# Kernel optimization log

Hardware: AMD Instinct MI355X
Metric: run time of the kernel (lower is better)

The kernel has to match this reference:

```python
import jax, jax.numpy as jnp
import numpy as np

B, N, C = 8, 1024, 768
H = 12
HD = C // H  # 64
SCALE = C ** (-0.5)  # NOTE: source scales by n_emb^-0.5, not head_dim^-0.5


def setup_inputs() -> dict:
    key = jax.random.key(0)
    k1, k2, k3 = jax.random.split(key, 3)
    x = jax.random.normal(k1, (B, N, C), dtype=jnp.float32)
    W_qkv = jax.random.normal(k2, (C, 3 * C), dtype=jnp.float32) * (C ** -0.5)
    b_qkv = jnp.zeros((3 * C,), dtype=jnp.float32)
    W_proj = jax.random.normal(k3, (C, C), dtype=jnp.float32) * (C ** -0.5)
    b_proj = jnp.zeros((C,), dtype=jnp.float32)
    return {"x": x, "W_qkv": W_qkv, "b_qkv": b_qkv, "W_proj": W_proj, "b_proj": b_proj}


def reference(x, W_qkv, b_qkv, W_proj, b_proj):
    # qkv projection: (B,N,3C) -> (3,B,H,N,HD)
    qkv = x @ W_qkv + b_qkv
    qkv = qkv.reshape(B, N, 3, H, HD).transpose(2, 0, 3, 1, 4)
    q, k, v = qkv[0], qkv[1], qkv[2]
    # scaled dot-product attention (full N x N, as in source)
    attn = jnp.einsum("bhnd,bhmd->bhnm", q, k) * SCALE
    attn = jax.nn.softmax(attn, axis=-1)
    out = jnp.einsum("bhnm,bhmd->bhnd", attn, v)
    out = out.transpose(0, 2, 1, 3).reshape(B, N, C)
    return out @ W_proj + b_proj
```

## Files before the change

### kernel.cpp

```cpp
#include <hip/hip_runtime.h>
#include <hip/hip_bf16.h>
#include <stdint.h>

#define Bb 8
#define Nn_ 1024
#define Cc_ 768
#define Hh 12
#define HDd 64
#define BHh 96
#define SCALE_F 0.03608439182435161f
#define CL2F (0.03608439182435161f * 1.4426950408889634f)
#define THRRAW (3.0f / CL2F)

typedef __attribute__((ext_vector_type(4))) float f32x4;
typedef __attribute__((ext_vector_type(8))) __bf16 bf16x8;

__device__ __forceinline__ unsigned short f2bf(float f) {
  uint32_t u = __builtin_bit_cast(uint32_t, f);
  uint32_t r = (u + 0x7fffu + ((u >> 16) & 1u)) >> 16;
  return (unsigned short)r;
}

__device__ __forceinline__ uint32_t cvtpk(float a, float b) {
  uint32_t r;
  asm("v_cvt_pk_bf16_f32 %0, %1, %2" : "=v"(r) : "v"(a), "v"(b));
  return r;
}

__device__ __forceinline__ f32x4 mfma16(bf16x8 a, bf16x8 b, f32x4 c) {
  return __builtin_amdgcn_mfma_f32_16x16x32_bf16(a, b, c, 0, 0, 0);
}

typedef const __attribute__((address_space(1))) uint32_t* gas1_t;
typedef __attribute__((address_space(3))) uint32_t* las3_t;
__device__ __forceinline__ void gl_lds16(const void* g, void* l) {
  __builtin_amdgcn_global_load_lds((gas1_t)g, (las3_t)l, 16, 0, 0);
}

#define VMCNT(n) asm volatile("s_waitcnt vmcnt(" #n ")" ::: "memory")
#define SBAR() __builtin_amdgcn_s_barrier()
#define SCHED_FENCE() __builtin_amdgcn_sched_barrier(0)

__global__ void k_cvt_x(const float* __restrict__ x, unsigned short* __restrict__ xb, int n4) {
  int i = blockIdx.x * blockDim.x + threadIdx.x;
  if (i >= n4) return;
  float4 v = ((const float4*)x)[i];
  ushort4 o;
  o.x = f2bf(v.x); o.y = f2bf(v.y); o.z = f2bf(v.z); o.w = f2bf(v.w);
  ((ushort4*)xb)[i] = o;
}

template <int R, int CC>
__global__ void k_transpose(const float* __restrict__ src, unsigned short* __restrict__ dst) {
  __shared__ unsigned short tile[64][65];
  int c0 = blockIdx.x * 64;
  int r0 = blockIdx.y * 64;
  int t = threadIdx.x;
#pragma unroll
  for (int i = 0; i < 16; ++i) {
    int idx = t + 256 * i;
    int r = idx >> 6, c = idx & 63;
    tile[r][c] = f2bf(src[(size_t)(r0 + r) * CC + c0 + c]);
  }
  __syncthreads();
#pragma unroll
  for (int i = 0; i < 16; ++i) {
    int idx = t + 256 * i;
    int a = idx >> 6, bq = idx & 63;
    dst[(size_t)(c0 + a) * R + r0 + bq] = tile[bq][a];
  }
}

__global__ __launch_bounds__(256) void k_transpose_v(const unsigned short* __restrict__ V,
                                                     unsigned short* __restrict__ Vt) {
  __shared__ unsigned short tile[64][72];
  int bh = blockIdx.y;
  int n0 = blockIdx.x * 64;
  int t = threadIdx.x;
  const unsigned short* src = V + ((size_t)bh * 1024 + n0) * 64;
#pragma unroll
  for (int i = 0; i < 4; ++i) {
    int idx = t + i * 256;
    int r = idx >> 4, c4 = idx & 15;
    ushort4 v = ((const ushort4*)src)[idx];
    tile[r][c4 * 4 + 0] = v.x; tile[r][c4 * 4 + 1] = v.y;
    tile[r][c4 * 4 + 2] = v.z; tile[r][c4 * 4 + 3] = v.w;
  }
  __syncthreads();
  unsigned short* dst = Vt + (size_t)bh * 64 * 1024 + n0;
#pragma unroll
  for (int i = 0; i < 4; ++i) {
    int idx = t + i * 256;
    int c = idx >> 4, n4 = idx & 15;
    ushort4 o;
    o.x = tile[n4 * 4 + 0][c]; o.y = tile[n4 * 4 + 1][c];
    o.z = tile[n4 * 4 + 2][c]; o.w = tile[n4 * 4 + 3][c];
    ((ushort4*)(dst + (size_t)c * 1024))[n4] = o;
  }
}

template <int EPI, int BMt, int BNt, int MINB>
__global__ __launch_bounds__(256, MINB) void k_gemm(
    const unsigned short* __restrict__ A, const unsigned short* __restrict__ Bt,
    const float* __restrict__ bias, float* __restrict__ out,
    unsigned short* __restrict__ Qb, unsigned short* __restrict__ Kb,
    unsigned short* __restrict__ Vb, int Nw) {
  constexpr int WGM = (BNt == 128) ? 2 : 4;
  constexpr int WM = BMt / WGM;
  constexpr int MR = WM / 16;
  constexpr int AL = BMt / 32;
  constexpr int BL = BNt / 32;
  constexpr int ASZ = BMt * 128;
  constexpr int BUFSZ = ASZ + BNt * 128;
  __shared__ char smem[2 * BUFSZ];
  int t = threadIdx.x;
  int w = t >> 6, lane = t & 63;
  int g = lane >> 4, l15 = lane & 15;
  int bid = blockIdx.x;
  int m0 = ((bid & 7) * 8 + ((bid >> 3) & 7)) * BMt;
  int n0 = (bid >> 6) * BNt;
  int wr = (BNt == 128) ? (w >> 1) : w;
  int wc = (BNt == 128) ? (w & 1) : 0;

  f32x4 acc[MR][4] = {};

  const char* gA[AL];
  const char* gB[BL];
  int sA[AL], sB[BL];
#pragma unroll
  for (int it = 0; it < AL; ++it) {
    int off = it * 4096 + t * 16;
    int row = off >> 7;
    int sb = (off & 127) ^ ((row & 7) << 4);
    gA[it] = (const char*)A + (size_t)(m0 + row) * 1536 + sb;
    sA[it] = it * 4096 + w * 1024;
  }
#pragma unroll
  for (int it = 0; it < BL; ++it) {
    int off = it * 4096 + t * 16;
    int row = off >> 7;
    int sb = (off & 127) ^ ((row & 7) << 4);
    gB[it] = (const char*)Bt + (size_t)(n0 + row) * 1536 + sb;
    sB[it] = ASZ + it * 4096 + w * 1024;
  }

  auto STG = [&](int buf, int kt) {
    char* base = smem + buf * BUFSZ;
#pragma unroll
    for (int it = 0; it < AL; ++it) gl_lds16(gA[it] + kt * 128, base + sA[it]);
#pragma unroll
    for (int it = 0; it < BL; ++it) gl_lds16(gB[it] + kt * 128, base + sB[it]);
  };

  const char *pa[2][MR], *pb[2][4];
#pragma unroll
  for (int ks = 0; ks < 2; ++ks) {
    int kb = ks * 64 + g * 16;
#pragma unroll
    for (int mi = 0; mi < MR; ++mi) {
      int rowA = wr * WM + mi * 16 + l15;
      pa[ks][mi] = smem + rowA * 128 + (kb ^ ((rowA & 7) << 4));
    }
#pragma unroll
    for (int ni = 0; ni < 4; ++ni) {
      int rowB = wc * 64 + ni * 16 + l15;
      pb[ks][ni] = smem + ASZ + rowB * 128 + (kb ^ ((rowB & 7) << 4));
    }
  }

  STG(0, 0);
#pragma unroll
  for (int kt = 0; kt < 12; ++kt) {
    int off = (kt & 1) * BUFSZ;
    if (kt < 11) {
      STG((kt & 1) ^ 1, kt + 1);
      if constexpr (BL == 4) { VMCNT(8); } else { VMCNT(6); }
    } else {
      VMCNT(0);
    }
    SBAR();
    SCHED_FENCE();
    bf16x8 av[2][MR], bv[2][4];
#pragma unroll
    for (int ks = 0; ks < 2; ++ks) {
#pragma unroll
      for (int mi = 0; mi < MR; ++mi) av[ks][mi] = *(const bf16x8*)(pa[ks][mi] + off);
#pragma unroll
      for (int ni = 0; ni < 4; ++ni) bv[ks][ni] = *(const bf16x8*)(pb[ks][ni] + off);
    }
#pragma unroll
    for (int ks = 0; ks < 2; ++ks)
#pragma unroll
      for (int mi = 0; mi < MR; ++mi)
#pragma unroll
        for (int ni = 0; ni < 4; ++ni)
          acc[mi][ni] = mfma16(av[ks][mi], bv[ks][ni], acc[mi][ni]);
    SCHED_FENCE();
    if (kt < 11) SBAR();
  }

#pragma unroll
  for (int mi = 0; mi < MR; ++mi) {
#pragma unroll
    for (int ni = 0; ni < 4; ++ni) {
      int col = n0 + wc * 64 + ni * 16 + l15;
      float bvs = bias[col];
#pragma unroll
      for (int j = 0; j < 4; ++j) {
        int row = m0 + wr * WM + mi * 16 + g * 4 + j;
        float val = acc[mi][ni][j] + bvs;
        if constexpr (EPI == 0) {
          out[(size_t)row * Nw + col] = val;
        } else {
          int bI = row >> 10, n = row & 1023;
          int typ = col / 768, within = col % 768;
          int h = within >> 6, d = within & 63;
          int bh = bI * 12 + h;
          unsigned short bf = f2bf(val);
          unsigned short* dst = (typ == 0) ? Qb : (typ == 1) ? Kb : Vb;
          dst[((size_t)bh * 1024 + n) * 64 + d] = bf;
        }
      }
    }
  }
}

__global__ __launch_bounds__(256, 3) void k_attn(
    const unsigned short* __restrict__ Q, const unsigned short* __restrict__ K,
    const unsigned short* __restrict__ Vt, unsigned short* __restrict__ Oa) {
  __shared__ char smem[49152];
  char* Ks = smem;
  char* Ps = smem + 32768;
  int t = threadIdx.x, w = t >> 6, lane = t & 63;
  int g = lane >> 4, l15 = lane & 15;

  int fb = blockIdx.x;
  int bh = (fb & 7) * 12 + ((fb >> 3) % 12);
  int n0 = (fb / 96) * 128;
  int bI = bh / 12, h = bh % 12;
  char* Pw = Ps + w * 4096;

  bf16x8 qf[2][2];
  {
    const char* qbase = (const char*)Q + ((size_t)bh * 1024 + n0 + w * 32 + l15) * 128 + g * 16;
    qf[0][0] = *(const bf16x8*)(qbase);
    qf[0][1] = *(const bf16x8*)(qbase + 64);
    qf[1][0] = *(const bf16x8*)(qbase + 16 * 128);
    qf[1][1] = *(const bf16x8*)(qbase + 16 * 128 + 64);
  }

  f32x4 acc[2][4] = {};
  float mrun[2] = {-INFINITY, -INFINITY};
  float lrun[2] = {0.f, 0.f};

  const char* pK[2][4];
#pragma unroll
  for (int ks = 0; ks < 2; ++ks)
#pragma unroll
    for (int ff = 0; ff < 4; ++ff) {
      int row = ff * 16 + l15;
      pK[ks][ff] = Ks + row * 128 + ((ks * 64 + g * 16) ^ ((row & 7) << 4));
    }
  char* pPw[2][4];
  const char* pPr[2][2];
#pragma unroll
  for (int q = 0; q < 2; ++q) {
    int prow = q * 16 + l15, swz = (l15 & 7) << 4;
#pragma unroll
    for (int ff = 0; ff < 4; ++ff) pPw[q][ff] = Pw + prow * 128 + ((ff * 32 + g * 8) ^ swz);
#pragma unroll
    for (int ks = 0; ks < 2; ++ks) pPr[q][ks] = Pw + prow * 128 + ((ks * 64 + g * 16) ^ swz);
  }

  int o0 = t * 16, o1 = t * 16 + 4096;
  int r0 = o0 >> 7, r1 = o1 >> 7;
  int sb0 = (o0 & 127) ^ ((r0 & 7) << 4);
  int sb1 = (o1 & 127) ^ ((r1 & 7) << 4);
  const char* KgA = (const char*)K + (size_t)bh * 131072 + (size_t)r0 * 128 + sb0;
  const char* KgB = (const char*)K + (size_t)bh * 131072 + (size_t)r1 * 128 + sb1;
  const char* VgA = (const char*)Vt + (size_t)bh * 131072 + (size_t)r0 * 2048 + sb0;
  const char* VgB = (const char*)Vt + (size_t)bh * 131072 + (size_t)r1 * 2048 + sb1;

  auto STG = [&](int buf, int mt) {
    char* Kd = Ks + buf * 8192;
    char* Vd = Ks + 16384 + buf * 8192;
    gl_lds16(KgA + (size_t)mt * 8192, Kd + w * 1024);
    gl_lds16(KgB + (size_t)mt * 8192, Kd + 4096 + w * 1024);
    gl_lds16(VgA + (size_t)mt * 128, Vd + w * 1024);
    gl_lds16(VgB + (size_t)mt * 128, Vd + 4096 + w * 1024);
  };

  auto TILE = [&](int off) {
    f32x4 s[4][2] = {};
#pragma unroll
    for (int ks = 0; ks < 2; ++ks)
#pragma unroll
      for (int ff = 0; ff < 4; ++ff) {
        bf16x8 kv = *(const bf16x8*)(pK[ks][ff] + off);
        s[ff][0] = mfma16(kv, qf[0][ks], s[ff][0]);
        s[ff][1] = mfma16(kv, qf[1][ks], s[ff][1]);
      }

    float pmax[2];
#pragma unroll
    for (int q = 0; q < 2; ++q) {
      float a0 = fmaxf(fmaxf(s[0][q][0], s[0][q][1]), fmaxf(s[0][q][2], s[0][q][3]));
      float a1 = fmaxf(fmaxf(s[1][q][0], s[1][q][1]), fmaxf(s[1][q][2], s[1][q][3]));
      float a2 = fmaxf(fmaxf(s[2][q][0], s[2][q][1]), fmaxf(s[2][q][2], s[2][q][3]));
      float a3 = fmaxf(fmaxf(s[3][q][0], s[3][q][1]), fmaxf(s[3][q][2], s[3][q][3]));
      float pm = fmaxf(fmaxf(a0, a1), fmaxf(a2, a3));
      pm = fmaxf(pm, __shfl_xor(pm, 16, 64));
      pm = fmaxf(pm, __shfl_xor(pm, 32, 64));
      pmax[q] = pm;
    }

    bool upd = (pmax[0] > mrun[0] + THRRAW) || (pmax[1] > mrun[1] + THRRAW);
    if (__any(upd)) {
#pragma unroll
      for (int q = 0; q < 2; ++q) {
        float mnew = fmaxf(mrun[q], pmax[q]);
        float alpha = __builtin_amdgcn_exp2f((mrun[q] - mnew) * CL2F);
        mrun[q] = mnew;
        lrun[q] *= alpha;
#pragma unroll
        for (int j = 0; j < 4; ++j) {
          float aj = __shfl(alpha, g * 4 + j, 64);
          acc[q][0][j] *= aj; acc[q][1][j] *= aj;
          acc[q][2][j] *= aj; acc[q][3][j] *= aj;
        }
      }
    }

#pragma unroll
    for (int q = 0; q < 2; ++q) {
      float nm = -mrun[q] * CL2F;
      float rs = 0.f;
#pragma unroll
      for (int ff = 0; ff < 4; ++ff) {
        float p0 = __builtin_amdgcn_exp2f(fmaf(s[ff][q][0], CL2F, nm));
        float p1 = __builtin_amdgcn_exp2f(fmaf(s[ff][q][1], CL2F, nm));
        float p2 = __builtin_amdgcn_exp2f(fmaf(s[ff][q][2], CL2F, nm));
        float p3 = __builtin_amdgcn_exp2f(fmaf(s[ff][q][3], CL2F, nm));
        rs += (p0 + p1) + (p2 + p3);
        uint2 pk;
        pk.x = cvtpk(p0, p1);
        pk.y = cvtpk(p2, p3);
        *(uint2*)(pPw[q][ff]) = pk;
      }
      rs += __shfl_xor(rs, 16, 64);
      rs += __shfl_xor(rs, 32, 64);
      lrun[q] += rs;
    }

#pragma unroll
    for (int ks = 0; ks < 2; ++ks) {
      bf16x8 pa0 = *(const bf16x8*)(pPr[0][ks]);
      bf16x8 pa1 = *(const bf16x8*)(pPr[1][ks]);
#pragma unroll
      for (int fd = 0; fd < 4; ++fd) {
        bf16x8 vv = *(const bf16x8*)(pK[ks][fd] + 16384 + off);
        acc[0][fd] = mfma16(pa0, vv, acc[0][fd]);
        acc[1][fd] = mfma16(pa1, vv, acc[1][fd]);
      }
    }
  };

  STG(0, 0);
  for (int mt2 = 0; mt2 < 8; ++mt2) {
    STG(1, 2 * mt2 + 1);
    VMCNT(4);
    SBAR();
    SCHED_FENCE();
    TILE(0);
    SCHED_FENCE();
    SBAR();
    if (mt2 < 7) {
      STG(0, 2 * mt2 + 2);
      VMCNT(4);
    } else {
      VMCNT(0);
    }
    SBAR();
    SCHED_FENCE();
    TILE(8192);
    SCHED_FENCE();
    if (mt2 < 7) SBAR();
  }

#pragma unroll
  for (int q = 0; q < 2; ++q) {
#pragma unroll
    for (int j = 0; j < 4; ++j) {
      float lv = __shfl(lrun[q], g * 4 + j, 64);
      float inv = 1.0f / lv;
      int n = n0 + w * 32 + q * 16 + g * 4 + j;
      size_t rowb = ((size_t)bI * 1024 + n) * 768 + h * 64;
#pragma unroll
      for (int fd = 0; fd < 4; ++fd)
        Oa[rowb + fd * 16 + l15] = (unsigned short)(cvtpk(acc[q][fd][j] * inv, 0.f) & 0xffffu);
    }
  }
}

extern "C" void kernel_launch(void* const* d_in, const int* in_sizes, int n_in,
                              void* d_out, int out_size, void* d_ws, size_t ws_size,
                              hipStream_t stream) {
  const float* x = (const float*)d_in[0];
  const float* Wqkv = (const float*)d_in[1];
  const float* bqkv = (const float*)d_in[2];
  const float* Wproj = (const float*)d_in[3];
  const float* bproj = (const float*)d_in[4];
  float* out = (float*)d_out;

  char* ws = (char*)d_ws;
  unsigned short* xb  = (unsigned short*)(ws);
  unsigned short* wqt = (unsigned short*)(ws + 12582912);
  unsigned short* wpt = (unsigned short*)(ws + 16121856);
  unsigned short* Qb  = (unsigned short*)(ws + 17301504);
  unsigned short* Kb  = (unsigned short*)(ws + 29884416);
  unsigned short* Vtb = (unsigned short*)(ws + 42467328);
  unsigned short* Oa  = (unsigned short*)(ws + 55050240);
  unsigned short* Vb  = Oa;

  k_cvt_x<<<dim3(6144), dim3(256), 0, stream>>>(x, xb, (Bb * Nn_ * Cc_) / 4);
  k_transpose<768, 2304><<<dim3(36, 12), dim3(256), 0, stream>>>(Wqkv, wqt);
  k_transpose<768, 768><<<dim3(12, 12), dim3(256), 0, stream>>>(Wproj, wpt);
  k_gemm<1, 128, 128, 2><<<dim3(1152), dim3(256), 0, stream>>>(xb, wqt, bqkv, nullptr,
                                                               Qb, Kb, Vb, 2304);
  k_transpose_v<<<dim3(16, 96), dim3(256), 0, stream>>>(Vb, Vtb);
  k_attn<<<dim3(768), dim3(256), 0, stream>>>(Qb, Kb, Vtb, Oa);
  k_gemm<0, 128, 64, 3><<<dim3(768), dim3(256), 0, stream>>>(Oa, wpt, bproj, out,
                                                             nullptr, nullptr, nullptr, 768);
}
```

Before: 113.3 us.

## Switch GEMM to triple-buffered LDS pipeline with half-depth K tiles

The GEMM kernel now stages K in 32-element (64-byte) chunks over 24 iterations, using three LDS buffers instead of two 128-byte double buffers. The LDS swizzle is adapted to the narrower rows. One barrier per iteration replaces two, and loads run two stages ahead. The smaller per-block LDS footprint lets launch bounds rise (2->3 and 3->4 blocks per CU) for more occupancy. The trade-off is more loop iterations and fewer MFMAs per barrier.

```diff
diff --git a/kernel.cpp b/kernel.cpp
--- a/kernel.cpp
+++ b/kernel.cpp
@@ -108,11 +108,12 @@
   constexpr int WGM = (BNt == 128) ? 2 : 4;
   constexpr int WM = BMt / WGM;
   constexpr int MR = WM / 16;
-  constexpr int AL = BMt / 32;
-  constexpr int BL = BNt / 32;
-  constexpr int ASZ = BMt * 128;
-  constexpr int BUFSZ = ASZ + BNt * 128;
-  __shared__ char smem[2 * BUFSZ];
+  constexpr int AL = BMt / 64;
+  constexpr int BL = BNt / 64;
+  constexpr int NLD = AL + BL;
+  constexpr int ASZ = BMt * 64;
+  constexpr int BUFSZ = ASZ + BNt * 64;
+  __shared__ char smem[3 * BUFSZ];
   int t = threadIdx.x;
   int w = t >> 6, lane = t & 63;
   int g = lane >> 4, l15 = lane & 15;
@@ -129,17 +130,17 @@
   int sA[AL], sB[BL];
 #pragma unroll
   for (int it = 0; it < AL; ++it) {
-    int off = it * 4096 + t * 16;
-    int row = off >> 7;
-    int sb = (off & 127) ^ ((row & 7) << 4);
+    int o = it * 4096 + t * 16;
+    int row = o >> 6;
+    int sb = (o & 63) ^ (((row >> 1) & 3) << 4);
     gA[it] = (const char*)A + (size_t)(m0 + row) * 1536 + sb;
     sA[it] = it * 4096 + w * 1024;
   }
 #pragma unroll
   for (int it = 0; it < BL; ++it) {
-    int off = it * 4096 + t * 16;
-    int row = off >> 7;
-    int sb = (off & 127) ^ ((row & 7) << 4);
+    int o = it * 4096 + t * 16;
+    int row = o >> 6;
+    int sb = (o & 63) ^ (((row >> 1) & 3) << 4);
     gB[it] = (const char*)Bt + (size_t)(n0 + row) * 1536 + sb;
     sB[it] = ASZ + it * 4096 + w * 1024;
   }
@@ -147,56 +148,49 @@
   auto STG = [&](int buf, int kt) {
     char* base = smem + buf * BUFSZ;
 #pragma unroll
-    for (int it = 0; it < AL; ++it) gl_lds16(gA[it] + kt * 128, base + sA[it]);
-#pragma unroll
-    for (int it = 0; it < BL; ++it) gl_lds16(gB[it] + kt * 128, base + sB[it]);
+    for (int it = 0; it < AL; ++it) gl_lds16(gA[it] + kt * 64, base + sA[it]);
+#pragma unroll
+    for (int it = 0; it < BL; ++it) gl_lds16(gB[it] + kt * 64, base + sB[it]);
   };
 
-  const char *pa[2][MR], *pb[2][4];
-#pragma unroll
-  for (int ks = 0; ks < 2; ++ks) {
-    int kb = ks * 64 + g * 16;
-#pragma unroll
-    for (int mi = 0; mi < MR; ++mi) {
-      int rowA = wr * WM + mi * 16 + l15;
-      pa[ks][mi] = smem + rowA * 128 + (kb ^ ((rowA & 7) << 4));
-    }
-#pragma unroll
-    for (int ni = 0; ni < 4; ++ni) {
-      int rowB = wc * 64 + ni * 16 + l15;
-      pb[ks][ni] = smem + ASZ + rowB * 128 + (kb ^ ((rowB & 7) << 4));
-    }
+  int swzr = ((l15 >> 1) & 3) << 4;
+  const char* pa[MR];
+  const char* pb[4];
+#pragma unroll
+  for (int mi = 0; mi < MR; ++mi) {
+    int rowA = wr * WM + mi * 16 + l15;
+    pa[mi] = smem + rowA * 64 + ((g * 16) ^ swzr);
+  }
+#pragma unroll
+  for (int ni = 0; ni < 4; ++ni) {
+    int rowB = wc * 64 + ni * 16 + l15;
+    pb[ni] = smem + ASZ + rowB * 64 + ((g * 16) ^ swzr);
   }
 
   STG(0, 0);
-#pragma unroll
-  for (int kt = 0; kt < 12; ++kt) {
-    int off = (kt & 1) * BUFSZ;
-    if (kt < 11) {
-      STG((kt & 1) ^ 1, kt + 1);
-      if constexpr (BL == 4) { VMCNT(8); } else { VMCNT(6); }
+  STG(1, 1);
+#pragma unroll
+  for (int kt = 0; kt < 24; ++kt) {
+    if (kt < 23) {
+      if constexpr (NLD == 4) { VMCNT(4); } else { VMCNT(3); }
     } else {
       VMCNT(0);
     }
     SBAR();
     SCHED_FENCE();
-    bf16x8 av[2][MR], bv[2][4];
-#pragma unroll
-    for (int ks = 0; ks < 2; ++ks) {
-#pragma unroll
-      for (int mi = 0; mi < MR; ++mi) av[ks][mi] = *(const bf16x8*)(pa[ks][mi] + off);
-#pragma unroll
-      for (int ni = 0; ni < 4; ++ni) bv[ks][ni] = *(const bf16x8*)(pb[ks][ni] + off);
-    }
-#pragma unroll
-    for (int ks = 0; ks < 2; ++ks)
-#pragma unroll
-      for (int mi = 0; mi < MR; ++mi)
-#pragma unroll
-        for (int ni = 0; ni < 4; ++ni)
-          acc[mi][ni] = mfma16(av[ks][mi], bv[ks][ni], acc[mi][ni]);
-    SCHED_FENCE();
-    if (kt < 11) SBAR();
+    if (kt + 2 < 24) STG((kt + 2) % 3, kt + 2);
+    int off = (kt % 3) * BUFSZ;
+    bf16x8 av[MR], bv[4];
+#pragma unroll
+    for (int mi = 0; mi < MR; ++mi) av[mi] = *(const bf16x8*)(pa[mi] + off);
+#pragma unroll
+    for (int ni = 0; ni < 4; ++ni) bv[ni] = *(const bf16x8*)(pb[ni] + off);
+#pragma unroll
+    for (int mi = 0; mi < MR; ++mi)
+#pragma unroll
+      for (int ni = 0; ni < 4; ++ni)
+        acc[mi][ni] = mfma16(av[mi], bv[ni], acc[mi][ni]);
+    SCHED_FENCE();
   }
 
 #pragma unroll
@@ -425,10 +419,10 @@
   k_cvt_x<<<dim3(6144), dim3(256), 0, stream>>>(x, xb, (Bb * Nn_ * Cc_) / 4);
   k_transpose<768, 2304><<<dim3(36, 12), dim3(256), 0, stream>>>(Wqkv, wqt);
   k_transpose<768, 768><<<dim3(12, 12), dim3(256), 0, stream>>>(Wproj, wpt);
-  k_gemm<1, 128, 128, 2><<<dim3(1152), dim3(256), 0, stream>>>(xb, wqt, bqkv, nullptr,
+  k_gemm<1, 128, 128, 3><<<dim3(1152), dim3(256), 0, stream>>>(xb, wqt, bqkv, nullptr,
                                                                Qb, Kb, Vb, 2304);
   k_transpose_v<<<dim3(16, 96), dim3(256), 0, stream>>>(Vb, Vtb);
   k_attn<<<dim3(768), dim3(256), 0, stream>>>(Qb, Kb, Vtb, Oa);
-  k_gemm<0, 128, 64, 3><<<dim3(768), dim3(256), 0, stream>>>(Oa, wpt, bproj, out,
+  k_gemm<0, 128, 64, 4><<<dim3(768), dim3(256), 0, stream>>>(Oa, wpt, bproj, out,
                                                              nullptr, nullptr, nullptr, 768);
 }
```

Result: slower. 122.7 us (+8.3%).
